# Kernel optimization log

Measured on AMD Instinct MI355X. Metric: run time of the kernel, lower is better.

The kernel has to match this reference:

```python
import jax, jax.numpy as jnp
import numpy as np

EPS = 1e-5
SCALE = 30.0

def _ln(x, g, b):
    mu = jnp.mean(x, -1, keepdims=True)
    var = jnp.mean((x - mu) ** 2, -1, keepdims=True)
    return (x - mu) / jnp.sqrt(var + EPS) * g + b

def _gather_nodes(h_V, E_idx):
    # h_V: [B,N,H], E_idx: [B,N,K] -> [B,N,K,H]
    return jax.vmap(lambda v, i: v[i])(h_V, E_idx)

def setup_inputs() -> dict:
    B, N, K, H, IN = 4, 2048, 48, 128, 128
    key = jax.random.key(0)
    ks = jax.random.split(key, 24)
    def lin(k, din, dout):
        kw, kb = jax.random.split(k)
        return (jax.random.normal(kw, (din, dout), jnp.float32) * 0.02,
                jax.random.normal(kb, (dout,), jnp.float32) * 0.02)
    W1_w, W1_b = lin(ks[0], H + IN, H)
    W2_w, W2_b = lin(ks[1], H, H)
    W3_w, W3_b = lin(ks[2], H, H)
    W11_w, W11_b = lin(ks[3], 2 * H + IN, H)
    W12_w, W12_b = lin(ks[4], H, H)
    W13_w, W13_b = lin(ks[5], H, IN)
    Win_w, Win_b = lin(ks[6], H, 4 * H)
    Wout_w, Wout_b = lin(ks[7], 4 * H, H)
    return {
        'h_V': jax.random.normal(ks[8], (B, N, H), jnp.float32),
        'h_E': jax.random.normal(ks[9], (B, N, K, IN), jnp.float32),
        'mask_V': jnp.ones((B, N), jnp.float32),
        'E_idx': jax.random.randint(ks[10], (B, N, K), 0, N),
        'mask_attend': jax.random.uniform(ks[11], (B, N, K), jnp.float32),
        'W1_w': W1_w, 'W1_b': W1_b, 'W2_w': W2_w, 'W2_b': W2_b,
        'W3_w': W3_w, 'W3_b': W3_b,
        'W11_w': W11_w, 'W11_b': W11_b, 'W12_w': W12_w, 'W12_b': W12_b,
        'W13_w': W13_w, 'W13_b': W13_b,
        'Win_w': Win_w, 'Win_b': Win_b, 'Wout_w': Wout_w, 'Wout_b': Wout_b,
        'ln1_g': jnp.ones((H,), jnp.float32), 'ln1_b': jnp.zeros((H,), jnp.float32),
        'ln2_g': jnp.ones((H,), jnp.float32), 'ln2_b': jnp.zeros((H,), jnp.float32),
        'ln3_g': jnp.ones((IN,), jnp.float32), 'ln3_b': jnp.zeros((IN,), jnp.float32),
    }

def reference(h_V, h_E, mask_V, E_idx, mask_attend,
              W1_w, W1_b, W2_w, W2_b, W3_w, W3_b,
              W11_w, W11_b, W12_w, W12_b, W13_w, W13_b,
              Win_w, Win_b, Wout_w, Wout_b,
              ln1_g, ln1_b, ln2_g, ln2_b, ln3_g, ln3_b):
    K = h_E.shape[-2]
    gelu = jax.nn.gelu
    # node message MLP over concat([h_V expanded, h_E])
    h_V_exp = jnp.broadcast_to(h_V[:, :, None, :], h_E.shape[:3] + (h_V.shape[-1],))
    h_EV = jnp.concatenate([h_V_exp, h_E], -1)  # [B,N,K,H+IN]
    h_msg = gelu(h_EV @ W1_w + W1_b)
    h_msg = gelu(h_msg @ W2_w + W2_b)
    h_msg = h_msg @ W3_w + W3_b
    h_msg = mask_attend[..., None] * h_msg
    dh = jnp.sum(h_msg, -2) / SCALE
    h_V = _ln(h_V + dh, ln1_g, ln1_b)  # dropout is identity in eval
    # FFN
    dh = gelu(h_V @ Win_w + Win_b) @ Wout_w + Wout_b
    h_V = _ln(h_V + dh, ln2_g, ln2_b)
    h_V = mask_V[..., None] * h_V
    # edge update: cat_neighbors_nodes = cat([h_E, gather(h_V, E_idx)], -1)
    h_nbr = _gather_nodes(h_V, E_idx)  # [B,N,K,H]
    h_EV2 = jnp.concatenate([h_E, h_nbr], -1)  # [B,N,K,IN+H]
    h_V_exp2 = jnp.broadcast_to(h_V[:, :, None, :], (h_V.shape[0], h_V.shape[1], K, h_V.shape[-1]))
    h_EV2 = jnp.concatenate([h_V_exp2, h_EV2], -1)  # [B,N,K,2H+IN]
    h_msg2 = gelu(h_EV2 @ W11_w + W11_b)
    h_msg2 = gelu(h_msg2 @ W12_w + W12_b)
    h_msg2 = h_msg2 @ W13_w + W13_b
    h_E = _ln(h_E + h_msg2, ln3_g, ln3_b)
    return (h_V, h_E)
```

## Files before the change

kernel.cpp:

```cpp
#include <hip/hip_runtime.h>
#include <stdint.h>


typedef __attribute__((ext_vector_type(8))) short bf16x8;
typedef __attribute__((ext_vector_type(4))) float f32x4;
typedef __attribute__((ext_vector_type(4))) float vf4;
typedef __attribute__((ext_vector_type(2))) float vf2;

#define MFMA16(a,b,c) __builtin_amdgcn_mfma_f32_16x16x32_bf16((a),(b),(c),0,0,0)
#define PITCH 17

__device__ __forceinline__ float bf2f(uint16_t u){
  union { uint32_t i; float f; } v; v.i = ((uint32_t)u) << 16; return v.f;
}
__device__ __forceinline__ uint32_t cvtpk(float lo, float hi){
  uint32_t r; asm("v_cvt_pk_bf16_f32 %0, %1, %2" : "=v"(r) : "v"(lo), "v"(hi));
  return r;
}
__device__ __forceinline__ uint16_t f2bf1(float x){ return (uint16_t)cvtpk(x, x); }
__device__ __forceinline__ uint4 pk8v(vf4 a, vf4 b){
  uint4 v; v.x=cvtpk(a[0],a[1]); v.y=cvtpk(a[2],a[3]);
  v.z=cvtpk(b[0],b[1]); v.w=cvtpk(b[2],b[3]); return v;
}
__device__ __forceinline__ float geluf(float x){
  float u = 0.7978845608028654f * x * fmaf(0.044715f, x*x, 1.0f);
  float e = __builtin_amdgcn_exp2f(2.8853900817779268f * u);
  float r = __builtin_amdgcn_rcpf(1.0f + e);
  return fmaf(-x, r, x);
}
template<int CTRL>
__device__ __forceinline__ float dpp_add(float x){
  int s = __builtin_amdgcn_update_dpp(0, __builtin_bit_cast(int, x), CTRL, 0xF, 0xF, true);
  return x + __builtin_bit_cast(float, s);
}
__device__ __forceinline__ float red16(float x){
  x = dpp_add<0x121>(x); x = dpp_add<0x122>(x);
  x = dpp_add<0x124>(x); x = dpp_add<0x128>(x);
  return x;
}
__device__ __forceinline__ bf16x8 wfragf(const float* __restrict__ W, int ncols,
                                         int k0, int col, int g){
  const float* p = W + (size_t)(k0 + g*8)*ncols + col;
  bf16x8 f;
#pragma unroll
  for (int j=0;j<8;j++) f[j] = (short)f2bf1(p[j*ncols]);
  return f;
}
__device__ __forceinline__ bf16x8 afrag(const uint4* tile, int row, int s, int g){
  return *(const bf16x8*)&tile[row*PITCH + 4*s + g];
}
__device__ __forceinline__ void st_m(uint4* tile, int row, int col, uint16_t val){
  ((uint16_t*)tile)[row*(PITCH*8) + col] = val;
}

__global__ __launch_bounds__(512) void k_pre(
  const float* __restrict__ hV, const float* __restrict__ W1,
  float* __restrict__ hvW1)
{
  const int tid = threadIdx.x;
  const int w = tid>>6, lane = tid&63, g = lane>>4, l15 = lane&15;
  const int col = w*16 + l15;
  const int node0 = blockIdx.x*16;
  bf16x8 Wf[4], A[4];
#pragma unroll
  for (int s=0;s<4;s++) Wf[s] = wfragf(W1,128,32*s,col,g);
#pragma unroll
  for (int s=0;s<4;s++){
    const float* p = hV + (size_t)(node0 + l15)*128 + 32*s + 8*g;
    uint4 t = pk8v(*(const vf4*)p, *(const vf4*)(p+4));
    A[s] = __builtin_bit_cast(bf16x8, t);
  }
  f32x4 acc = {0,0,0,0};
#pragma unroll
  for (int s=0;s<4;s++) acc = MFMA16(A[s], Wf[s], acc);
#pragma unroll
  for (int r=0;r<4;r++) hvW1[(size_t)(node0 + 4*g + r)*128 + col] = acc[r];
}

__global__ __launch_bounds__(512) void k_node(
  const float* __restrict__ hV, const float* __restrict__ hE,
  const float* __restrict__ mAtt, const float* __restrict__ hvW1,
  const float* __restrict__ W1, const float* __restrict__ B1,
  const float* __restrict__ W2, const float* __restrict__ B2,
  const float* __restrict__ W3, const float* __restrict__ B3,
  const float* __restrict__ LG1, const float* __restrict__ LB1,
  uint16_t* __restrict__ x1b)
{
  __shared__ uint4 Ab[2][48*PITCH];
  __shared__ uint4 Cb[48*PITCH];
  __shared__ float maskb[48];
  __shared__ float dhb[128];

  const int tid = threadIdx.x;
  const int w = tid >> 6, lane = tid & 63, g = lane >> 4, l15 = lane & 15;
  const int col = w*16 + l15;
  const int row0 = tid>>4, cir = tid&15, row1 = 32 + (tid>>4);

  bf16x8 W1e[4], W2f[4], W3f[4];
#pragma unroll
  for (int s=0;s<4;s++) W1e[s] = wfragf(W1,128,128+32*s,col,g);
#pragma unroll
  for (int s=0;s<4;s++) W2f[s] = wfragf(W2,128,32*s,col,g);
#pragma unroll
  for (int s=0;s<4;s++) W3f[s] = wfragf(W3,128,32*s,col,g);
  const float b1c = B1[col], b2c = B2[col], b3c = B3[col];
  float lg0 = 0, lg1 = 0, lb0 = 0, lb1 = 0;
  if (tid < 64){ lg0 = LG1[2*tid]; lg1 = LG1[2*tid+1]; lb0 = LB1[2*tid]; lb1 = LB1[2*tid+1]; }

  vf4 sr0, sr1, sr2, sr3; float mk = 0.f, hv1;
  {
    const int node = blockIdx.x*8;
    const float* hb = hE + (size_t)node*6144;
    sr0 = __builtin_nontemporal_load((const vf4*)(hb + tid*8));
    sr1 = __builtin_nontemporal_load((const vf4*)(hb + tid*8 + 4));
    if (tid < 256){
      sr2 = __builtin_nontemporal_load((const vf4*)(hb + 4096 + tid*8));
      sr3 = __builtin_nontemporal_load((const vf4*)(hb + 4096 + tid*8 + 4));
    }
    if (tid >= 64 && tid < 112) mk = mAtt[(size_t)node*48 + (tid-64)];
    hv1 = hvW1[(size_t)node*128 + col];
    Ab[0][row0*PITCH + cir] = pk8v(sr0, sr1);
    if (tid < 256) Ab[0][row1*PITCH + cir] = pk8v(sr2, sr3);
    if (tid >= 64 && tid < 112) maskb[tid-64] = mk;
  }
  __syncthreads();

  for (int it=0; it<8; ++it){
    const int node = blockIdx.x*8 + it;
    const uint4* Ac = Ab[it&1];
    uint4* Acm = Ab[it&1];
    uint4* An  = Ab[(it&1)^1];
    f32x4 ahv = {hv1, hv1, hv1, hv1};
#pragma unroll
    for (int t=0;t<3;t++){
      f32x4 acc = ahv;
      int row = 16*t + l15;
#pragma unroll
      for (int s=0;s<4;s++) acc = MFMA16(afrag(Ac,row,s,g), W1e[s], acc);
#pragma unroll
      for (int r=0;r<4;r++) st_m(Cb, 16*t+4*g+r, col, f2bf1(geluf(acc[r]+b1c)));
    }
    __syncthreads();
#pragma unroll
    for (int t=0;t<3;t++){
      f32x4 acc = {0,0,0,0};
      int row = 16*t + l15;
#pragma unroll
      for (int s=0;s<4;s++) acc = MFMA16(afrag(Cb,row,s,g), W2f[s], acc);
#pragma unroll
      for (int r=0;r<4;r++) st_m(Acm, 16*t+4*g+r, col, f2bf1(geluf(acc[r]+b2c)));
    }
    __syncthreads();
    if (it < 7){
      const float* hb = hE + (size_t)(node+1)*6144;
      sr0 = __builtin_nontemporal_load((const vf4*)(hb + tid*8));
      sr1 = __builtin_nontemporal_load((const vf4*)(hb + tid*8 + 4));
      if (tid < 256){
        sr2 = __builtin_nontemporal_load((const vf4*)(hb + 4096 + tid*8));
        sr3 = __builtin_nontemporal_load((const vf4*)(hb + 4096 + tid*8 + 4));
      }
      if (tid >= 64 && tid < 112) mk = mAtt[(size_t)(node+1)*48 + (tid-64)];
      hv1 = hvW1[(size_t)(node+1)*128 + col];
    }
    float pp = 0.f;
#pragma unroll
    for (int t=0;t<3;t++){
      f32x4 acc = {0,0,0,0};
      int row = 16*t + l15;
#pragma unroll
      for (int s=0;s<4;s++) acc = MFMA16(afrag(Ac,row,s,g), W3f[s], acc);
#pragma unroll
      for (int r=0;r<4;r++) pp += maskb[16*t+4*g+r] * (acc[r] + b3c);
    }
    pp += __shfl_xor(pp, 16);
    pp += __shfl_xor(pp, 32);
    if (lane < 16) dhb[col] = pp * (1.f/30.f);
    __syncthreads();
    if (tid < 64){
      int c0 = 2*tid, c1 = c0+1;
      float2 hv2 = *(const float2*)(hV + (size_t)node*128 + c0);
      float xa = hv2.x + dhb[c0];
      float xc = hv2.y + dhb[c1];
      float s1 = xa + xc, s2 = xa*xa + xc*xc;
      s1 = red16(s1); s2 = red16(s2);
      s1 += __shfl_xor(s1,16); s2 += __shfl_xor(s2,16);
      s1 += __shfl_xor(s1,32); s2 += __shfl_xor(s2,32);
      float mu = s1 * (1.0f/128.0f);
      float var = fmaxf(s2 * (1.0f/128.0f) - mu*mu, 0.f);
      float rstd = __builtin_amdgcn_rsqf(var + 1e-5f);
      float ya = (xa-mu)*rstd*lg0 + lb0;
      float yc = (xc-mu)*rstd*lg1 + lb1;
      ((uint32_t*)x1b)[(size_t)node*64 + tid] = cvtpk(ya, yc);
    }
    if (it < 7){
      An[row0*PITCH + cir] = pk8v(sr0, sr1);
      if (tid < 256) An[row1*PITCH + cir] = pk8v(sr2, sr3);
      if (tid >= 64 && tid < 112) maskb[tid-64] = mk;
    }
    __syncthreads();
  }
}

template<bool HV11>
__global__ __launch_bounds__(512) void k_ffn(
  const uint16_t* __restrict__ x1b,
  const float* __restrict__ Win, const float* __restrict__ Bin,
  const float* __restrict__ Wout, const float* __restrict__ Bout,
  const float* __restrict__ W11,
  const float* __restrict__ LG2, const float* __restrict__ LB2,
  const float* __restrict__ maskV,
  float* __restrict__ outV, uint16_t* __restrict__ outVb,
  float* __restrict__ hvW11)
{
  __shared__ uint4 lh[16*65];
  __shared__ float xb[16*129];

  const int tid = threadIdx.x;
  const int w = tid>>6, lane = tid&63, g = lane>>4, l15 = lane&15;
  const int colo = w*16 + l15;

  bf16x8 WiF[4][4], WoF[16], W11s[4];
#pragma unroll
  for (int s=0;s<4;s++)
#pragma unroll
    for (int c=0;c<4;c++) WiF[s][c] = wfragf(Win,512,32*s, w*64 + c*16 + l15, g);
#pragma unroll
  for (int s=0;s<16;s++) WoF[s] = wfragf(Wout,128,32*s, colo, g);
  if (HV11){
#pragma unroll
    for (int s=0;s<4;s++) W11s[s] = wfragf(W11,128,32*s,colo,g);
  }
  float binc[4];
#pragma unroll
  for (int c=0;c<4;c++) binc[c] = Bin[w*64 + c*16 + l15];
  const float boutc = Bout[colo];
  const float lg0 = LG2[2*lane], lg1 = LG2[2*lane+1];
  const float lb0 = LB2[2*lane], lb1 = LB2[2*lane+1];

  for (int it=0; it<2; ++it){
    const int node0 = (blockIdx.x*2 + it)*16;
    bf16x8 A[4];
#pragma unroll
    for (int s=0;s<4;s++) A[s] = *(const bf16x8*)(x1b + (size_t)(node0 + l15)*128 + 32*s + 8*g);
#pragma unroll
    for (int c=0;c<4;c++){
      f32x4 acc = {0,0,0,0};
#pragma unroll
      for (int s=0;s<4;s++) acc = MFMA16(A[s], WiF[s][c], acc);
      int colh = w*64 + c*16 + l15;
#pragma unroll
      for (int r=0;r<4;r++){
        int row = 4*g + r;
        ((uint16_t*)lh)[row*(65*8) + colh] = f2bf1(geluf(acc[r] + binc[c]));
      }
    }
    __syncthreads();
    f32x4 acc = {0,0,0,0};
#pragma unroll
    for (int s=0;s<16;s++){
      bf16x8 a = *(const bf16x8*)&lh[l15*65 + 4*s + g];
      acc = MFMA16(a, WoF[s], acc);
    }
#pragma unroll
    for (int r=0;r<4;r++){
      int row = 4*g + r;
      xb[row*129 + colo] = bf2f(x1b[(size_t)(node0+row)*128 + colo]) + acc[r] + boutc;
    }
    __syncthreads();
#pragma unroll
    for (int rr=0; rr<2; ++rr){
      int row = w + rr*8;
      int c0 = 2*lane;
      float xa = xb[row*129 + c0], xc = xb[row*129 + c0 + 1];
      float s1 = xa + xc, s2 = xa*xa + xc*xc;
      s1 = red16(s1); s2 = red16(s2);
      s1 += __shfl_xor(s1,16); s2 += __shfl_xor(s2,16);
      s1 += __shfl_xor(s1,32); s2 += __shfl_xor(s2,32);
      float mu = s1*(1.0f/128.0f);
      float var = fmaxf(s2*(1.0f/128.0f)-mu*mu, 0.f);
      float rstd = __builtin_amdgcn_rsqf(var + 1e-5f);
      float mv = maskV[node0 + row];
      float ya = ((xa-mu)*rstd*lg0 + lb0) * mv;
      float yc = ((xc-mu)*rstd*lg1 + lb1) * mv;
      vf2 o2; o2[0] = ya; o2[1] = yc;
      __builtin_nontemporal_store(o2, (vf2*)outV + (size_t)(node0+row)*64 + lane);
      uint32_t pk = cvtpk(ya, yc);
      if (outVb)
        ((uint32_t*)outVb)[(size_t)(node0+row)*64 + lane] = pk;
      if (HV11)
        ((uint32_t*)lh)[row*132 + lane] = pk;
    }
    __syncthreads();
    if (HV11){
      f32x4 a2 = {0,0,0,0};
#pragma unroll
      for (int s=0;s<4;s++){
        bf16x8 a = *(const bf16x8*)&((uint32_t*)lh)[l15*132 + 16*s + 4*g];
        a2 = MFMA16(a, W11s[s], a2);
      }
#pragma unroll
      for (int r=0;r<4;r++)
        hvW11[(size_t)(node0 + 4*g + r)*128 + colo] = a2[r];
      __syncthreads();
    }
  }
}

__global__ __launch_bounds__(512) void k_edge_fast(
  const float* __restrict__ hE, const int* __restrict__ Eidx,
  const uint16_t* __restrict__ hV2b, const float* __restrict__ hvW11,
  const float* __restrict__ W11, const float* __restrict__ B11,
  const float* __restrict__ W12, const float* __restrict__ B12,
  const float* __restrict__ W13, const float* __restrict__ B13,
  const float* __restrict__ LG3, const float* __restrict__ LB3,
  float* __restrict__ outE)
{
  __shared__ uint4 Ab[2][48*PITCH];
  __shared__ uint4 Bb[48*PITCH];
  __shared__ uint4 Cb[48*PITCH];

  const int tid = threadIdx.x;
  const int w = tid>>6, lane = tid&63, g = lane>>4, l15 = lane&15;
  const int col = w*16 + l15;
  const int row0 = tid>>4, cir = tid&15, row1 = 32 + (tid>>4);

  bf16x8 W11e[4], W11n[4], W12f[4], W13f[4];
#pragma unroll
  for (int s=0;s<4;s++) W11e[s] = wfragf(W11,128, 128+32*s,col,g);
#pragma unroll
  for (int s=0;s<4;s++) W11n[s] = wfragf(W11,128, 256+32*s,col,g);
#pragma unroll
  for (int s=0;s<4;s++) W12f[s] = wfragf(W12,128,     32*s,col,g);
#pragma unroll
  for (int s=0;s<4;s++) W13f[s] = wfragf(W13,128,     32*s,col,g);
  const float b11c = B11[col], b12c = B12[col], b13c = B13[col];
  const float lg0 = LG3[2*lane], lg1 = LG3[2*lane+1];
  const float lb0 = LB3[2*lane], lb1 = LB3[2*lane+1];

  vf4 sr0, sr1, sr2, sr3; int gi0, gi1; float hv11;
  {
    const int node = blockIdx.x*8;
    const int bb = (node >> 11) << 11;
    const float* hb = hE + (size_t)node*6144;
    sr0 = __builtin_nontemporal_load((const vf4*)(hb + tid*8));
    sr1 = __builtin_nontemporal_load((const vf4*)(hb + tid*8 + 4));
    if (tid < 256){
      sr2 = __builtin_nontemporal_load((const vf4*)(hb + 4096 + tid*8));
      sr3 = __builtin_nontemporal_load((const vf4*)(hb + 4096 + tid*8 + 4));
    }
    gi0 = Eidx[(size_t)node*48 + (tid>>4)];
    gi1 = (tid < 256) ? Eidx[(size_t)node*48 + 32 + (tid>>4)] : 0;
    hv11 = hvW11[(size_t)node*128 + col];
    uint4 gq0 = *(const uint4*)(hV2b + (size_t)(bb + gi0)*128 + (tid&15)*8);
    uint4 gq1;
    if (tid < 256) gq1 = *(const uint4*)(hV2b + (size_t)(bb + gi1)*128 + (tid&15)*8);
    Ab[0][row0*PITCH + cir] = pk8v(sr0, sr1);
    Bb[row0*PITCH + cir] = gq0;
    if (tid < 256){
      Ab[0][row1*PITCH + cir] = pk8v(sr2, sr3);
      Bb[row1*PITCH + cir] = gq1;
    }
  }
  __syncthreads();

  for (int it=0; it<8; ++it){
    const int node = blockIdx.x*8 + it;
    const uint4* Ac = Ab[it&1];
    uint4* An = Ab[(it&1)^1];
    f32x4 ahv = {hv11, hv11, hv11, hv11};
#pragma unroll
    for (int t=0;t<3;t++){
      f32x4 acc = ahv;
      int row = 16*t + l15;
#pragma unroll
      for (int s=0;s<4;s++) acc = MFMA16(afrag(Ac,row,s,g), W11e[s], acc);
#pragma unroll
      for (int s=0;s<4;s++) acc = MFMA16(afrag(Bb,row,s,g), W11n[s], acc);
#pragma unroll
      for (int r=0;r<4;r++) st_m(Cb, 16*t+4*g+r, col, f2bf1(geluf(acc[r]+b11c)));
    }
    __syncthreads();
#pragma unroll
    for (int t=0;t<3;t++){
      f32x4 acc = {0,0,0,0};
      int row = 16*t + l15;
#pragma unroll
      for (int s=0;s<4;s++) acc = MFMA16(afrag(Cb,row,s,g), W12f[s], acc);
#pragma unroll
      for (int r=0;r<4;r++) st_m(Bb, 16*t+4*g+r, col, f2bf1(geluf(acc[r]+b12c)));
    }
    __syncthreads();
    if (it < 7){
      const float* hb = hE + (size_t)(node+1)*6144;
      sr0 = __builtin_nontemporal_load((const vf4*)(hb + tid*8));
      sr1 = __builtin_nontemporal_load((const vf4*)(hb + tid*8 + 4));
      if (tid < 256){
        sr2 = __builtin_nontemporal_load((const vf4*)(hb + 4096 + tid*8));
        sr3 = __builtin_nontemporal_load((const vf4*)(hb + 4096 + tid*8 + 4));
      }
      gi0 = Eidx[(size_t)(node+1)*48 + (tid>>4)];
      gi1 = (tid < 256) ? Eidx[(size_t)(node+1)*48 + 32 + (tid>>4)] : 0;
      hv11 = hvW11[(size_t)(node+1)*128 + col];
    }
#pragma unroll
    for (int t=0;t<3;t++){
      f32x4 acc = {0,0,0,0};
      int row = 16*t + l15;
#pragma unroll
      for (int s=0;s<4;s++) acc = MFMA16(afrag(Bb,row,s,g), W13f[s], acc);
#pragma unroll
      for (int r=0;r<4;r++) st_m(Cb, 16*t+4*g+r, col, f2bf1(acc[r]+b13c));
    }
    __syncthreads();
    uint4 gq0, gq1;
    if (it < 7){
      const int bb2 = ((node+1) >> 11) << 11;
      gq0 = *(const uint4*)(hV2b + (size_t)(bb2 + gi0)*128 + (tid&15)*8);
      if (tid < 256) gq1 = *(const uint4*)(hV2b + (size_t)(bb2 + gi1)*128 + (tid&15)*8);
    }
#pragma unroll
    for (int rr=0; rr<6; ++rr){
      int row = w + rr*8;
      int c0 = 2*lane;
      uint32_t pe = ((const uint32_t*)Ac)[row*(PITCH*4) + lane];
      uint32_t pv = ((const uint32_t*)Cb)[row*(PITCH*4) + lane];
      float xa = bf2f((uint16_t)(pe & 0xffff)) + bf2f((uint16_t)(pv & 0xffff));
      float xc = bf2f((uint16_t)(pe >> 16))    + bf2f((uint16_t)(pv >> 16));
      float s1 = xa + xc, s2 = xa*xa + xc*xc;
      s1 = red16(s1); s2 = red16(s2);
      s1 += __shfl_xor(s1,16); s2 += __shfl_xor(s2,16);
      s1 += __shfl_xor(s1,32); s2 += __shfl_xor(s2,32);
      float mu = s1*(1.0f/128.0f);
      float var = fmaxf(s2*(1.0f/128.0f)-mu*mu, 0.f);
      float rstd = __builtin_amdgcn_rsqf(var+1e-5f);
      float ya = (xa-mu)*rstd*lg0 + lb0;
      float yc = (xc-mu)*rstd*lg1 + lb1;
      vf2 o2; o2[0] = ya; o2[1] = yc;
      __builtin_nontemporal_store(o2, (vf2*)outE + ((size_t)node*48 + row)*64 + lane);
    }
    if (it < 7){
      An[row0*PITCH + cir] = pk8v(sr0, sr1);
      Bb[row0*PITCH + cir] = gq0;
      if (tid < 256){
        An[row1*PITCH + cir] = pk8v(sr2, sr3);
        Bb[row1*PITCH + cir] = gq1;
      }
    }
    __syncthreads();
  }
}

__global__ __launch_bounds__(512) void k_edge_safe(
  const float* __restrict__ hE, const int* __restrict__ Eidx,
  const float* __restrict__ hV2f,
  const float* __restrict__ W11, const float* __restrict__ B11,
  const float* __restrict__ W12, const float* __restrict__ B12,
  const float* __restrict__ W13, const float* __restrict__ B13,
  const float* __restrict__ LG3, const float* __restrict__ LB3,
  float* __restrict__ outE)
{
  __shared__ uint4 Ab[2][48*PITCH];
  __shared__ uint4 Bb[48*PITCH];
  __shared__ uint4 Cb[48*PITCH];
  __shared__ uint4 hvb[16];

  const int tid = threadIdx.x;
  const int w = tid>>6, lane = tid&63, g = lane>>4, l15 = lane&15;
  const int col = w*16 + l15;
  const int row0 = tid>>4, cir = tid&15, row1 = 32 + (tid>>4);

  bf16x8 Ws[4], W11e[4], W11n[4], W12f[4], W13f[4];
#pragma unroll
  for (int s=0;s<4;s++) Ws[s]   = wfragf(W11,128,     32*s,col,g);
#pragma unroll
  for (int s=0;s<4;s++) W11e[s] = wfragf(W11,128, 128+32*s,col,g);
#pragma unroll
  for (int s=0;s<4;s++) W11n[s] = wfragf(W11,128, 256+32*s,col,g);
#pragma unroll
  for (int s=0;s<4;s++) W12f[s] = wfragf(W12,128,     32*s,col,g);
#pragma unroll
  for (int s=0;s<4;s++) W13f[s] = wfragf(W13,128,     32*s,col,g);
  const float b11c = B11[col], b12c = B12[col], b13c = B13[col];

  vf4 sr0, sr1, sr2, sr3; int gi0, gi1; uint4 hvr;
  {
    const int node = blockIdx.x*8;
    const int bb = (node >> 11) << 11;
    const float* hb = hE + (size_t)node*6144;
    sr0 = __builtin_nontemporal_load((const vf4*)(hb + tid*8));
    sr1 = __builtin_nontemporal_load((const vf4*)(hb + tid*8 + 4));
    if (tid < 256){
      sr2 = __builtin_nontemporal_load((const vf4*)(hb + 4096 + tid*8));
      sr3 = __builtin_nontemporal_load((const vf4*)(hb + 4096 + tid*8 + 4));
    }
    gi0 = Eidx[(size_t)node*48 + (tid>>4)];
    gi1 = (tid < 256) ? Eidx[(size_t)node*48 + 32 + (tid>>4)] : 0;
    uint4 gq0, gq1;
    {
      const float* p0 = hV2f + (size_t)(bb + gi0)*128 + (tid&15)*8;
      gq0 = pk8v(*(const vf4*)p0, *(const vf4*)(p0+4));
      if (tid < 256){
        const float* p1 = hV2f + (size_t)(bb + gi1)*128 + (tid&15)*8;
        gq1 = pk8v(*(const vf4*)p1, *(const vf4*)(p1+4));
      }
      if (tid < 16){
        const float* p = hV2f + (size_t)node*128 + tid*8;
        hvr = pk8v(*(const vf4*)p, *(const vf4*)(p+4));
      }
    }
    Ab[0][row0*PITCH + cir] = pk8v(sr0, sr1);
    Bb[row0*PITCH + cir] = gq0;
    if (tid < 256){
      Ab[0][row1*PITCH + cir] = pk8v(sr2, sr3);
      Bb[row1*PITCH + cir] = gq1;
    }
    if (tid < 16) hvb[tid] = hvr;
  }
  __syncthreads();

  for (int it=0; it<8; ++it){
    const int node = blockIdx.x*8 + it;
    const uint4* Ac = Ab[it&1];
    uint4* An = Ab[(it&1)^1];
    f32x4 ahv = {0,0,0,0};
#pragma unroll
    for (int s=0;s<4;s++) ahv = MFMA16(*(const bf16x8*)&hvb[4*s+g], Ws[s], ahv);
#pragma unroll
    for (int t=0;t<3;t++){
      f32x4 acc = ahv;
      int row = 16*t + l15;
#pragma unroll
      for (int s=0;s<4;s++) acc = MFMA16(afrag(Ac,row,s,g), W11e[s], acc);
#pragma unroll
      for (int s=0;s<4;s++) acc = MFMA16(afrag(Bb,row,s,g), W11n[s], acc);
#pragma unroll
      for (int r=0;r<4;r++) st_m(Cb, 16*t+4*g+r, col, f2bf1(geluf(acc[r]+b11c)));
    }
    __syncthreads();
#pragma unroll
    for (int t=0;t<3;t++){
      f32x4 acc = {0,0,0,0};
      int row = 16*t + l15;
#pragma unroll
      for (int s=0;s<4;s++) acc = MFMA16(afrag(Cb,row,s,g), W12f[s], acc);
#pragma unroll
      for (int r=0;r<4;r++) st_m(Bb, 16*t+4*g+r, col, f2bf1(geluf(acc[r]+b12c)));
    }
    __syncthreads();
    if (it < 7){
      const float* hb = hE + (size_t)(node+1)*6144;
      sr0 = __builtin_nontemporal_load((const vf4*)(hb + tid*8));
      sr1 = __builtin_nontemporal_load((const vf4*)(hb + tid*8 + 4));
      if (tid < 256){
        sr2 = __builtin_nontemporal_load((const vf4*)(hb + 4096 + tid*8));
        sr3 = __builtin_nontemporal_load((const vf4*)(hb + 4096 + tid*8 + 4));
      }
      gi0 = Eidx[(size_t)(node+1)*48 + (tid>>4)];
      gi1 = (tid < 256) ? Eidx[(size_t)(node+1)*48 + 32 + (tid>>4)] : 0;
    }
#pragma unroll
    for (int t=0;t<3;t++){
      f32x4 acc = {0,0,0,0};
      int row = 16*t + l15;
#pragma unroll
      for (int s=0;s<4;s++) acc = MFMA16(afrag(Bb,row,s,g), W13f[s], acc);
#pragma unroll
      for (int r=0;r<4;r++) st_m(Cb, 16*t+4*g+r, col, f2bf1(acc[r]+b13c));
    }
    __syncthreads();
    uint4 gq0, gq1;
    if (it < 7){
      const int bb2 = ((node+1) >> 11) << 11;
      const float* p0 = hV2f + (size_t)(bb2 + gi0)*128 + (tid&15)*8;
      gq0 = pk8v(*(const vf4*)p0, *(const vf4*)(p0+4));
      if (tid < 256){
        const float* p1 = hV2f + (size_t)(bb2 + gi1)*128 + (tid&15)*8;
        gq1 = pk8v(*(const vf4*)p1, *(const vf4*)(p1+4));
      }
      if (tid < 16){
        const float* p = hV2f + (size_t)(node+1)*128 + tid*8;
        hvr = pk8v(*(const vf4*)p, *(const vf4*)(p+4));
      }
    }
#pragma unroll
    for (int rr=0; rr<6; ++rr){
      int row = w + rr*8;
      int c0 = 2*lane;
      uint32_t pe = ((const uint32_t*)Ac)[row*(PITCH*4) + lane];
      uint32_t pv = ((const uint32_t*)Cb)[row*(PITCH*4) + lane];
      float xa = bf2f((uint16_t)(pe & 0xffff)) + bf2f((uint16_t)(pv & 0xffff));
      float xc = bf2f((uint16_t)(pe >> 16))    + bf2f((uint16_t)(pv >> 16));
      float s1 = xa + xc, s2 = xa*xa + xc*xc;
      s1 = red16(s1); s2 = red16(s2);
      s1 += __shfl_xor(s1,16); s2 += __shfl_xor(s2,16);
      s1 += __shfl_xor(s1,32); s2 += __shfl_xor(s2,32);
      float mu = s1*(1.0f/128.0f);
      float var = fmaxf(s2*(1.0f/128.0f)-mu*mu, 0.f);
      float rstd = __builtin_amdgcn_rsqf(var+1e-5f);
      float ya = (xa-mu)*rstd*LG3[c0] + LB3[c0];
      float yc = (xc-mu)*rstd*LG3[c0+1] + LB3[c0+1];
      vf2 o2; o2[0] = ya; o2[1] = yc;
      __builtin_nontemporal_store(o2, (vf2*)outE + ((size_t)node*48 + row)*64 + lane);
    }
    if (it < 7){
      An[row0*PITCH + cir] = pk8v(sr0, sr1);
      Bb[row0*PITCH + cir] = gq0;
      if (tid < 256){
        An[row1*PITCH + cir] = pk8v(sr2, sr3);
        Bb[row1*PITCH + cir] = gq1;
      }
      if (tid < 16) hvb[tid] = hvr;
    }
    __syncthreads();
  }
}

extern "C" void kernel_launch(void* const* d_in, const int* in_sizes, int n_in,
                              void* d_out, int out_size, void* d_ws, size_t ws_size,
                              hipStream_t stream){
  const float* hV   = (const float*)d_in[0];
  const float* hE   = (const float*)d_in[1];
  const float* mV   = (const float*)d_in[2];
  const int*   Eidx = (const int*)d_in[3];
  const float* mAtt = (const float*)d_in[4];
  const float* W1 = (const float*)d_in[5];  const float* B1 = (const float*)d_in[6];
  const float* W2 = (const float*)d_in[7];  const float* B2 = (const float*)d_in[8];
  const float* W3 = (const float*)d_in[9];  const float* B3 = (const float*)d_in[10];
  const float* W11 = (const float*)d_in[11]; const float* B11 = (const float*)d_in[12];
  const float* W12 = (const float*)d_in[13]; const float* B12 = (const float*)d_in[14];
  const float* W13 = (const float*)d_in[15]; const float* B13 = (const float*)d_in[16];
  const float* Win = (const float*)d_in[17]; const float* Bin = (const float*)d_in[18];
  const float* Wout= (const float*)d_in[19]; const float* Bout= (const float*)d_in[20];
  const float* LG1 = (const float*)d_in[21]; const float* LB1 = (const float*)d_in[22];
  const float* LG2 = (const float*)d_in[23]; const float* LB2 = (const float*)d_in[24];
  const float* LG3 = (const float*)d_in[25]; const float* LB3 = (const float*)d_in[26];

  float* outV = (float*)d_out;
  float* outE = outV + (size_t)1048576;
  uint16_t* x1b = (uint16_t*)(outE + (size_t)1048576);
  float*    hvW1 = outE + (size_t)1572864;

  const bool bf16g = ws_size >= ((size_t)2<<20);
  const bool fast  = ws_size >= ((size_t)6<<20);
  uint16_t* outVb = bf16g ? (uint16_t*)d_ws : nullptr;
  float*    hvW11 = fast ? (float*)((char*)d_ws + ((size_t)2<<20)) : nullptr;

  hipLaunchKernelGGL(k_pre, dim3(512), dim3(512), 0, stream, hV, W1, hvW1);
  hipLaunchKernelGGL(k_node, dim3(1024), dim3(512), 0, stream,
      hV, hE, mAtt, hvW1, W1,B1, W2,B2, W3,B3, LG1,LB1, x1b);
  if (fast){
    hipLaunchKernelGGL((k_ffn<true>), dim3(256), dim3(512), 0, stream,
        x1b, Win,Bin, Wout,Bout, W11, LG2,LB2, mV, outV, outVb, hvW11);
    hipLaunchKernelGGL(k_edge_fast, dim3(1024), dim3(512), 0, stream,
        hE, Eidx, outVb, hvW11, W11,B11, W12,B12, W13,B13, LG3,LB3, outE);
  } else {
    hipLaunchKernelGGL((k_ffn<false>), dim3(256), dim3(512), 0, stream,
        x1b, Win,Bin, Wout,Bout, W11, LG2,LB2, mV, outV, nullptr, nullptr);
    hipLaunchKernelGGL(k_edge_safe, dim3(1024), dim3(512), 0, stream,
        hE, Eidx, outV, W11,B11, W12,B12, W13,B13, LG3,LB3, outE);
  }
}
```

Before: 318.0 us.

## Halve edge kernel block to 4 waves, each computing two column tiles

The edge kernel drops from 512 to 256 threads per block. Each wave now covers two 16-column output tiles, so it holds twice as many weight fragments in registers and reuses each loaded A fragment across both tiles. Global loads and LayerNorm rows are redistributed across the smaller block. This cuts LDS fragment reads per MFMA and halves the waves per block, at the cost of higher register pressure and less latency hiding per block.

```diff
diff --git a/kernel.cpp b/kernel.cpp
--- a/kernel.cpp
+++ b/kernel.cpp
@@ -306,7 +306,7 @@
   }
 }
 
-__global__ __launch_bounds__(512) void k_edge_fast(
+__global__ __launch_bounds__(256) void k_edge3(
   const float* __restrict__ hE, const int* __restrict__ Eidx,
   const uint16_t* __restrict__ hV2b, const float* __restrict__ hvW11,
   const float* __restrict__ W11, const float* __restrict__ B11,
@@ -321,44 +321,51 @@
 
   const int tid = threadIdx.x;
   const int w = tid>>6, lane = tid&63, g = lane>>4, l15 = lane&15;
-  const int col = w*16 + l15;
-  const int row0 = tid>>4, cir = tid&15, row1 = 32 + (tid>>4);
-
-  bf16x8 W11e[4], W11n[4], W12f[4], W13f[4];
-#pragma unroll
-  for (int s=0;s<4;s++) W11e[s] = wfragf(W11,128, 128+32*s,col,g);
-#pragma unroll
-  for (int s=0;s<4;s++) W11n[s] = wfragf(W11,128, 256+32*s,col,g);
-#pragma unroll
-  for (int s=0;s<4;s++) W12f[s] = wfragf(W12,128,     32*s,col,g);
-#pragma unroll
-  for (int s=0;s<4;s++) W13f[s] = wfragf(W13,128,     32*s,col,g);
-  const float b11c = B11[col], b12c = B12[col], b13c = B13[col];
+  const int col0 = w*16 + l15;
+  bf16x8 We[2][4], Wn[2][4], W2f[2][4], W3f[2][4];
+#pragma unroll
+  for (int h=0;h<2;h++){
+    int ch = col0 + 64*h;
+#pragma unroll
+    for (int s=0;s<4;s++){
+      We[h][s]  = wfragf(W11,128, 128+32*s, ch, g);
+      Wn[h][s]  = wfragf(W11,128, 256+32*s, ch, g);
+      W2f[h][s] = wfragf(W12,128,     32*s, ch, g);
+      W3f[h][s] = wfragf(W13,128,     32*s, ch, g);
+    }
+  }
+  const float b11a = B11[col0], b11q = B11[col0+64];
+  const float b12a = B12[col0], b12q = B12[col0+64];
+  const float b13a = B13[col0], b13q = B13[col0+64];
   const float lg0 = LG3[2*lane], lg1 = LG3[2*lane+1];
   const float lb0 = LB3[2*lane], lb1 = LB3[2*lane+1];
 
-  vf4 sr0, sr1, sr2, sr3; int gi0, gi1; float hv11;
+  vf4 sr[6]; int gi[3]; float hva, hvq;
   {
     const int node = blockIdx.x*8;
-    const int bb = (node >> 11) << 11;
+    const int bb = (node>>11)<<11;
     const float* hb = hE + (size_t)node*6144;
-    sr0 = __builtin_nontemporal_load((const vf4*)(hb + tid*8));
-    sr1 = __builtin_nontemporal_load((const vf4*)(hb + tid*8 + 4));
-    if (tid < 256){
-      sr2 = __builtin_nontemporal_load((const vf4*)(hb + 4096 + tid*8));
-      sr3 = __builtin_nontemporal_load((const vf4*)(hb + 4096 + tid*8 + 4));
-    }
-    gi0 = Eidx[(size_t)node*48 + (tid>>4)];
-    gi1 = (tid < 256) ? Eidx[(size_t)node*48 + 32 + (tid>>4)] : 0;
-    hv11 = hvW11[(size_t)node*128 + col];
-    uint4 gq0 = *(const uint4*)(hV2b + (size_t)(bb + gi0)*128 + (tid&15)*8);
-    uint4 gq1;
-    if (tid < 256) gq1 = *(const uint4*)(hV2b + (size_t)(bb + gi1)*128 + (tid&15)*8);
-    Ab[0][row0*PITCH + cir] = pk8v(sr0, sr1);
-    Bb[row0*PITCH + cir] = gq0;
-    if (tid < 256){
-      Ab[0][row1*PITCH + cir] = pk8v(sr2, sr3);
-      Bb[row1*PITCH + cir] = gq1;
+#pragma unroll
+    for (int q=0;q<3;q++){
+      int c = tid + 256*q;
+      sr[2*q]   = __builtin_nontemporal_load((const vf4*)(hb + (size_t)c*8));
+      sr[2*q+1] = __builtin_nontemporal_load((const vf4*)(hb + (size_t)c*8 + 4));
+      gi[q] = Eidx[(size_t)node*48 + (c>>4)];
+    }
+    hva = hvW11[(size_t)node*128 + col0];
+    hvq = hvW11[(size_t)node*128 + col0 + 64];
+    uint4 gq[3];
+#pragma unroll
+    for (int q=0;q<3;q++){
+      int c = tid + 256*q;
+      gq[q] = *(const uint4*)(hV2b + (size_t)(bb + gi[q])*128 + (c&15)*8);
+    }
+#pragma unroll
+    for (int q=0;q<3;q++){
+      int c = tid + 256*q;
+      int row = c>>4, cir = c&15;
+      Ab[0][row*PITCH + cir] = pk8v(sr[2*q], sr[2*q+1]);
+      Bb[row*PITCH + cir] = gq[q];
     }
   }
   __syncthreads();
@@ -367,61 +374,87 @@
     const int node = blockIdx.x*8 + it;
     const uint4* Ac = Ab[it&1];
     uint4* An = Ab[(it&1)^1];
-    f32x4 ahv = {hv11, hv11, hv11, hv11};
-#pragma unroll
-    for (int t=0;t<3;t++){
-      f32x4 acc = ahv;
-      int row = 16*t + l15;
-#pragma unroll
-      for (int s=0;s<4;s++) acc = MFMA16(afrag(Ac,row,s,g), W11e[s], acc);
-#pragma unroll
-      for (int s=0;s<4;s++) acc = MFMA16(afrag(Bb,row,s,g), W11n[s], acc);
-#pragma unroll
-      for (int r=0;r<4;r++) st_m(Cb, 16*t+4*g+r, col, f2bf1(geluf(acc[r]+b11c)));
-    }
-    __syncthreads();
-#pragma unroll
-    for (int t=0;t<3;t++){
-      f32x4 acc = {0,0,0,0};
-      int row = 16*t + l15;
-#pragma unroll
-      for (int s=0;s<4;s++) acc = MFMA16(afrag(Cb,row,s,g), W12f[s], acc);
-#pragma unroll
-      for (int r=0;r<4;r++) st_m(Bb, 16*t+4*g+r, col, f2bf1(geluf(acc[r]+b12c)));
+#pragma unroll
+    for (int t=0;t<3;t++){
+      int row = 16*t + l15;
+      bf16x8 ae[4], bn[4];
+#pragma unroll
+      for (int s=0;s<4;s++){ ae[s] = afrag(Ac,row,s,g); bn[s] = afrag(Bb,row,s,g); }
+#pragma unroll
+      for (int h=0;h<2;h++){
+        float hv = h ? hvq : hva;
+        f32x4 acc = {hv,hv,hv,hv};
+#pragma unroll
+        for (int s=0;s<4;s++) acc = MFMA16(ae[s], We[h][s], acc);
+#pragma unroll
+        for (int s=0;s<4;s++) acc = MFMA16(bn[s], Wn[h][s], acc);
+        float bs = h ? b11q : b11a;
+        int ch = col0 + 64*h;
+#pragma unroll
+        for (int r=0;r<4;r++) st_m(Cb, 16*t+4*g+r, ch, f2bf1(geluf(acc[r]+bs)));
+      }
+    }
+    __syncthreads();
+#pragma unroll
+    for (int t=0;t<3;t++){
+      int row = 16*t + l15;
+      bf16x8 a[4];
+#pragma unroll
+      for (int s=0;s<4;s++) a[s] = afrag(Cb,row,s,g);
+#pragma unroll
+      for (int h=0;h<2;h++){
+        f32x4 acc = {0,0,0,0};
+#pragma unroll
+        for (int s=0;s<4;s++) acc = MFMA16(a[s], W2f[h][s], acc);
+        float bs = h ? b12q : b12a;
+        int ch = col0 + 64*h;
+#pragma unroll
+        for (int r=0;r<4;r++) st_m(Bb, 16*t+4*g+r, ch, f2bf1(geluf(acc[r]+bs)));
+      }
     }
     __syncthreads();
     if (it < 7){
       const float* hb = hE + (size_t)(node+1)*6144;
-      sr0 = __builtin_nontemporal_load((const vf4*)(hb + tid*8));
-      sr1 = __builtin_nontemporal_load((const vf4*)(hb + tid*8 + 4));
-      if (tid < 256){
-        sr2 = __builtin_nontemporal_load((const vf4*)(hb + 4096 + tid*8));
-        sr3 = __builtin_nontemporal_load((const vf4*)(hb + 4096 + tid*8 + 4));
-      }
-      gi0 = Eidx[(size_t)(node+1)*48 + (tid>>4)];
-      gi1 = (tid < 256) ? Eidx[(size_t)(node+1)*48 + 32 + (tid>>4)] : 0;
-      hv11 = hvW11[(size_t)(node+1)*128 + col];
-    }
-#pragma unroll
-    for (int t=0;t<3;t++){
-      f32x4 acc = {0,0,0,0};
-      int row = 16*t + l15;
-#pragma unroll
-      for (int s=0;s<4;s++) acc = MFMA16(afrag(Bb,row,s,g), W13f[s], acc);
-#pragma unroll
-      for (int r=0;r<4;r++) st_m(Cb, 16*t+4*g+r, col, f2bf1(acc[r]+b13c));
-    }
-    __syncthreads();
-    uint4 gq0, gq1;
-    if (it < 7){
-      const int bb2 = ((node+1) >> 11) << 11;
-      gq0 = *(const uint4*)(hV2b + (size_t)(bb2 + gi0)*128 + (tid&15)*8);
-      if (tid < 256) gq1 = *(const uint4*)(hV2b + (size_t)(bb2 + gi1)*128 + (tid&15)*8);
-    }
-#pragma unroll
-    for (int rr=0; rr<6; ++rr){
-      int row = w + rr*8;
-      int c0 = 2*lane;
+#pragma unroll
+      for (int q=0;q<3;q++){
+        int c = tid + 256*q;
+        sr[2*q]   = __builtin_nontemporal_load((const vf4*)(hb + (size_t)c*8));
+        sr[2*q+1] = __builtin_nontemporal_load((const vf4*)(hb + (size_t)c*8 + 4));
+        gi[q] = Eidx[(size_t)(node+1)*48 + (c>>4)];
+      }
+      hva = hvW11[(size_t)(node+1)*128 + col0];
+      hvq = hvW11[(size_t)(node+1)*128 + col0 + 64];
+    }
+#pragma unroll
+    for (int t=0;t<3;t++){
+      int row = 16*t + l15;
+      bf16x8 a[4];
+#pragma unroll
+      for (int s=0;s<4;s++) a[s] = afrag(Bb,row,s,g);
+#pragma unroll
+      for (int h=0;h<2;h++){
+        f32x4 acc = {0,0,0,0};
+#pragma unroll
+        for (int s=0;s<4;s++) acc = MFMA16(a[s], W3f[h][s], acc);
+        float bs = h ? b13q : b13a;
+        int ch = col0 + 64*h;
+#pragma unroll
+        for (int r=0;r<4;r++) st_m(Cb, 16*t+4*g+r, ch, f2bf1(acc[r]+bs));
+      }
+    }
+    __syncthreads();
+    uint4 gq[3];
+    if (it < 7){
+      const int bb2 = ((node+1)>>11)<<11;
+#pragma unroll
+      for (int q=0;q<3;q++){
+        int c = tid + 256*q;
+        gq[q] = *(const uint4*)(hV2b + (size_t)(bb2 + gi[q])*128 + (c&15)*8);
+      }
+    }
+#pragma unroll
+    for (int rr=0; rr<12; ++rr){
+      int row = 4*rr + w;
       uint32_t pe = ((const uint32_t*)Ac)[row*(PITCH*4) + lane];
       uint32_t pv = ((const uint32_t*)Cb)[row*(PITCH*4) + lane];
       float xa = bf2f((uint16_t)(pe & 0xffff)) + bf2f((uint16_t)(pv & 0xffff));
@@ -439,11 +472,12 @@
       __builtin_nontemporal_store(o2, (vf2*)outE + ((size_t)node*48 + row)*64 + lane);
     }
     if (it < 7){
-      An[row0*PITCH + cir] = pk8v(sr0, sr1);
-      Bb[row0*PITCH + cir] = gq0;
-      if (tid < 256){
-        An[row1*PITCH + cir] = pk8v(sr2, sr3);
-        Bb[row1*PITCH + cir] = gq1;
+#pragma unroll
+      for (int q=0;q<3;q++){
+        int c = tid + 256*q;
+        int row = c>>4, cir = c&15;
+        An[row*PITCH + cir] = pk8v(sr[2*q], sr[2*q+1]);
+        Bb[row*PITCH + cir] = gq[q];
       }
     }
     __syncthreads();
@@ -651,7 +685,7 @@
   if (fast){
     hipLaunchKernelGGL((k_ffn<true>), dim3(256), dim3(512), 0, stream,
         x1b, Win,Bin, Wout,Bout, W11, LG2,LB2, mV, outV, outVb, hvW11);
-    hipLaunchKernelGGL(k_edge_fast, dim3(1024), dim3(512), 0, stream,
+    hipLaunchKernelGGL(k_edge3, dim3(1024), dim3(256), 0, stream,
         hE, Eidx, outVb, hvW11, W11,B11, W12,B12, W13,B13, LG3,LB3, outE);
   } else {
     hipLaunchKernelGGL((k_ffn<false>), dim3(256), dim3(512), 0, stream,
```

After: 353.5 us. +11.2%, slower.
